# Kernel tuning notes

Measured on AMD Instinct MI355X. Metric: run time of the kernel, lower is better.

Reference implementation:

```python
import jax, jax.numpy as jnp
import numpy as np

D_MODEL = 1024
N_HEADS = 16
D_HEAD = D_MODEL // N_HEADS
B, S = 4, 2048


def setup_inputs() -> dict:
    key = jax.random.key(0)
    ks = jax.random.split(key, 12)
    std = 1.0 / np.sqrt(D_MODEL)
    inp = {
        "q": jax.random.normal(ks[0], (B, S, D_MODEL), jnp.float32),
        "k": jax.random.normal(ks[1], (B, S, D_MODEL), jnp.float32),
        "v": jax.random.normal(ks[2], (B, S, D_MODEL), jnp.float32),
        # causal mask: 1 where attention is disallowed (j > i)
        "mask": jnp.triu(jnp.ones((S, S), jnp.int32), k=1)[None, None],
        "Wq": jax.random.normal(ks[3], (D_MODEL, D_MODEL), jnp.float32) * std,
        "bq": jnp.zeros((D_MODEL,), jnp.float32),
        "Wk": jax.random.normal(ks[4], (D_MODEL, D_MODEL), jnp.float32) * std,
        "bk": jnp.zeros((D_MODEL,), jnp.float32),
        "Wv": jax.random.normal(ks[5], (D_MODEL, D_MODEL), jnp.float32) * std,
        "bv": jnp.zeros((D_MODEL,), jnp.float32),
        "Wo": jax.random.normal(ks[6], (D_MODEL, D_MODEL), jnp.float32) * std,
        "bo": jnp.zeros((D_MODEL,), jnp.float32),
    }
    return inp


def _split_heads(x):
    # [B, S, D] -> [B, H, S, d_head]
    b, s, _ = x.shape
    return x.reshape(b, s, N_HEADS, D_HEAD).transpose(0, 2, 1, 3)


def reference(q, k, v, mask, Wq, bq, Wk, bk, Wv, bv, Wo, bo):
    # torch Linear: y = x @ W.T + b
    qh = _split_heads(q @ Wq.T + bq)
    kh = _split_heads(k @ Wk.T + bk)
    vh = _split_heads(v @ Wv.T + bv)
    # NOTE: original scales by sqrt(d_model), not sqrt(d_head)
    scale = 1.0 / np.sqrt(D_MODEL).astype(np.float32)
    logits = jnp.einsum("bhqd,bhkd->bhqk", qh, kh) * scale
    logits = logits + mask.astype(logits.dtype) * (-1e9)
    weights = jax.nn.softmax(logits, axis=-1)
    attn = jnp.einsum("bhqk,bhkd->bhqd", weights, vh)
    attn = attn.transpose(0, 2, 1, 3).reshape(q.shape[0], -1, D_MODEL)
    out = attn @ Wo.T + bo
    return out, weights
```

## Files before the change

kernel.cpp:

```cpp
#include <hip/hip_runtime.h>
#include <stdint.h>

typedef unsigned short u16;
typedef __attribute__((ext_vector_type(8))) short bf16x8;
typedef __attribute__((ext_vector_type(8))) unsigned short us8;
typedef __attribute__((ext_vector_type(4))) float f32x4;

typedef __attribute__((address_space(1))) void as1_void;
typedef __attribute__((address_space(3))) void as3_void;

#define S_LEN 2048
#define DMODEL 1024
#define DH 64
#define NHEADS 16
#define NB 4
#define GM (NB * S_LEN)
#define GN DMODEL
#define GK DMODEL
#define SCALE 0.03125f

__device__ __forceinline__ void gload16(const void* g, void* l) {
  __builtin_amdgcn_global_load_lds((const as1_void*)g, (as3_void*)l, 16, 0, 0);
}
__device__ __forceinline__ float bf2f(u16 u) {
  union { unsigned int i; float f; } x; x.i = ((unsigned int)u) << 16; return x.f;
}
__device__ __forceinline__ u16 f2bf(float f) {
  union { float f; unsigned int i; } x; x.f = f;
  unsigned int u = x.i + 0x7fffu + ((x.i >> 16) & 1u);
  return (u16)(u >> 16);
}
__device__ __forceinline__ f32x4 mfma16(bf16x8 a, bf16x8 b, f32x4 c) {
  return __builtin_amdgcn_mfma_f32_16x16x32_bf16(a, b, c, 0, 0, 0);
}
__device__ __forceinline__ void nt_store4(f32x4 v, float* p) {
  __builtin_nontemporal_store(v, (f32x4*)p);
}

__device__ __forceinline__ void cvt_chunk(const float* s, u16* d, int i) {
  const f32x4 a = *(const f32x4*)(s + (size_t)i * 8);
  const f32x4 b = *(const f32x4*)(s + (size_t)i * 8 + 4);
  us8 o;
  o[0] = f2bf(a[0]); o[1] = f2bf(a[1]); o[2] = f2bf(a[2]); o[3] = f2bf(a[3]);
  o[4] = f2bf(b[0]); o[5] = f2bf(b[1]); o[6] = f2bf(b[2]); o[7] = f2bf(b[3]);
  *(us8*)(d + (size_t)i * 8) = o;
}
__global__ __launch_bounds__(256)
void cvt3(const float* __restrict__ s0, const float* __restrict__ s1,
          const float* __restrict__ s2, u16* __restrict__ d0,
          u16* __restrict__ d1, u16* __restrict__ d2, int n8) {
  const int i = blockIdx.x * 256 + threadIdx.x;
  if (i >= n8) return;
  const float* s; u16* d;
  if (blockIdx.y == 0)      { s = s0; d = d0; }
  else if (blockIdx.y == 1) { s = s1; d = d1; }
  else                      { s = s2; d = d2; }
  cvt_chunk(s, d, i);
}
__global__ __launch_bounds__(256)
void cvt4(const float* __restrict__ s0, const float* __restrict__ s1,
          const float* __restrict__ s2, const float* __restrict__ s3,
          u16* __restrict__ d0, u16* __restrict__ d1,
          u16* __restrict__ d2, u16* __restrict__ d3, int n8) {
  const int i = blockIdx.x * 256 + threadIdx.x;
  if (i >= n8) return;
  const float* s; u16* d;
  if (blockIdx.y == 0)      { s = s0; d = d0; }
  else if (blockIdx.y == 1) { s = s1; d = d1; }
  else if (blockIdx.y == 2) { s = s2; d = d2; }
  else                      { s = s3; d = d3; }
  cvt_chunk(s, d, i);
}

template<bool OUTF>
__device__ __forceinline__ void gemm_body(const u16* __restrict__ A,
                                          const u16* __restrict__ W,
                                          const float* __restrict__ bias,
                                          void* __restrict__ Cv,
                                          u16* smem) {
  u16* As = smem;
  u16* Bs = smem + 2 * 8192;
  const int tid  = threadIdx.x;
  const int lane = tid & 63;
  const int wv   = tid >> 6;
  const int wr   = wv >> 1, wc = wv & 1;
  const int rlow = lane & 15, rhi = lane >> 4;
  const int m0 = blockIdx.x * 128;
  const int n0 = blockIdx.y * 128;

  f32x4 acc[4][4];
#pragma unroll
  for (int i = 0; i < 4; ++i)
#pragma unroll
    for (int j = 0; j < 4; ++j) acc[i][j] = (f32x4){0.f, 0.f, 0.f, 0.f};

#define STAGE_G(bufi, kk)                                                     \
  {                                                                           \
    _Pragma("unroll")                                                         \
    for (int i = 0; i < 4; ++i) {                                             \
      const int c = i * 256 + tid;                                            \
      const int row = c >> 3, cw = c & 7;                                     \
      const int koff = ((kk) << 6) + ((cw ^ (row & 7)) << 3);                 \
      gload16(A + (size_t)(m0 + row) * GK + koff,                             \
              &As[(bufi) * 8192 + ((c - lane) << 3)]);                        \
      gload16(W + (size_t)(n0 + row) * GK + koff,                             \
              &Bs[(bufi) * 8192 + ((c - lane) << 3)]);                        \
    }                                                                         \
  }

  const int nk = GK >> 6;
  STAGE_G(0, 0);
  __syncthreads();
  int buf = 0;
  for (int kk = 0; kk < nk; ++kk) {
    if (kk + 1 < nk) STAGE_G(buf ^ 1, kk + 1);
    const u16* Ab = &As[buf * 8192];
    const u16* Bb = &Bs[buf * 8192];
    bf16x8 af[4][2], bfr[4][2];
#pragma unroll
    for (int mi = 0; mi < 4; ++mi) {
      const int row = wr * 64 + mi * 16 + rlow;
#pragma unroll
      for (int k2 = 0; k2 < 2; ++k2)
        af[mi][k2] = *(const bf16x8*)&Ab[row * 64 + (((rhi + k2 * 4) ^ (row & 7)) << 3)];
    }
#pragma unroll
    for (int ni = 0; ni < 4; ++ni) {
      const int row = wc * 64 + ni * 16 + rlow;
#pragma unroll
      for (int k2 = 0; k2 < 2; ++k2)
        bfr[ni][k2] = *(const bf16x8*)&Bb[row * 64 + (((rhi + k2 * 4) ^ (row & 7)) << 3)];
    }
#pragma unroll
    for (int mi = 0; mi < 4; ++mi)
#pragma unroll
      for (int ni = 0; ni < 4; ++ni) {
        acc[mi][ni] = mfma16(af[mi][0], bfr[ni][0], acc[mi][ni]);
        acc[mi][ni] = mfma16(af[mi][1], bfr[ni][1], acc[mi][ni]);
      }
    __syncthreads();
    buf ^= 1;
  }
#undef STAGE_G

  if constexpr (OUTF) {
    float* Cs = (float*)smem;
#pragma unroll
    for (int ni = 0; ni < 4; ++ni) {
      const int col = wc * 64 + ni * 16 + rlow;
      const float bv = bias[n0 + col];
#pragma unroll
      for (int mi = 0; mi < 4; ++mi)
#pragma unroll
        for (int r = 0; r < 4; ++r)
          Cs[(wr * 64 + mi * 16 + rhi * 4 + r) * 128 + col] = acc[mi][ni][r] + bv;
    }
    __syncthreads();
#pragma unroll
    for (int i = 0; i < 16; ++i) {
      const int c = i * 256 + tid;
      const int row = c >> 5, cw = c & 31;
      const f32x4 t = *(const f32x4*)&Cs[row * 128 + cw * 4];
      nt_store4(t, &((float*)Cv)[(size_t)(m0 + row) * GN + n0 + cw * 4]);
    }
  } else {
    u16* Cs = smem;
#pragma unroll
    for (int ni = 0; ni < 4; ++ni) {
      const int col = wc * 64 + ni * 16 + rlow;
      const float bv = bias[n0 + col];
#pragma unroll
      for (int mi = 0; mi < 4; ++mi)
#pragma unroll
        for (int r = 0; r < 4; ++r)
          Cs[(wr * 64 + mi * 16 + rhi * 4 + r) * 144 + col] = f2bf(acc[mi][ni][r] + bv);
    }
    __syncthreads();
#pragma unroll
    for (int i = 0; i < 8; ++i) {
      const int c = i * 256 + tid;
      const int row = c >> 4, cw = c & 15;
      const us8 t = *(const us8*)&Cs[row * 144 + cw * 8];
      *(us8*)&((u16*)Cv)[(size_t)(m0 + row) * GN + n0 + cw * 8] = t;
    }
  }
}

__global__ __launch_bounds__(256, 2)
void gemm_qkv(const u16* __restrict__ xq, const u16* __restrict__ xk,
              const u16* __restrict__ xv, const u16* __restrict__ wq,
              const u16* __restrict__ wk, const u16* __restrict__ wv,
              const float* __restrict__ bq, const float* __restrict__ bk,
              const float* __restrict__ bv, u16* __restrict__ oq,
              u16* __restrict__ ok, u16* __restrict__ ov) {
  __shared__ u16 smem[4 * 8192];
  const u16 *A, *W; const float* bias; u16* C;
  if (blockIdx.z == 0)      { A = xq; W = wq; bias = bq; C = oq; }
  else if (blockIdx.z == 1) { A = xk; W = wk; bias = bk; C = ok; }
  else                      { A = xv; W = wv; bias = bv; C = ov; }
  gemm_body<false>(A, W, bias, C, smem);
}

__global__ __launch_bounds__(256, 2)
void gemm_o(const u16* __restrict__ A, const u16* __restrict__ W,
            const float* __restrict__ bias, float* __restrict__ C) {
  __shared__ u16 smem[4 * 8192];
  gemm_body<true>(A, W, bias, C, smem);
}

__global__ __launch_bounds__(512, 4)
void attn_fused(const u16* __restrict__ qh, const u16* __restrict__ kh,
                const u16* __restrict__ vh, float* __restrict__ wout,
                u16* __restrict__ am)
{
  __shared__ u16 smem[34304];
  u16* Ws = smem;
  u16* Qs = smem;
  u16* Ks = smem + 17408;
  u16* VT = smem + 17408 + 8192;

  const int tid = threadIdx.x, lane = tid & 63, wv = tid >> 6;
  const int rlow = lane & 15, rhi = lane >> 4;
  const int idx = blockIdx.x;
  const int bh  = idx & 63;
  const int qt  = 15 - (idx >> 6);
  const int b = bh >> 4, h = bh & 15;
  const int q0 = qt << 7;
  const size_t headoff = (size_t)b * S_LEN * DMODEL + h * DH;

#pragma unroll
  for (int i = 0; i < 2; ++i) {
    const int c = i * 512 + tid;
    const int row = c >> 3, cw = c & 7;
    gload16(qh + headoff + (size_t)(q0 + row) * DMODEL + ((cw ^ (row & 7)) << 3),
            &Qs[(c - lane) << 3]);
  }
  __syncthreads();
  bf16x8 qf[2];
  {
    const int row = wv * 16 + rlow;
#pragma unroll
    for (int k2 = 0; k2 < 2; ++k2)
      qf[k2] = *(const bf16x8*)&Qs[row * 64 + (((rhi + k2 * 4) ^ (row & 7)) << 3)];
  }

  const int gi_base = q0 + wv * 16 + rhi * 4;
  float ssum[4] = {0.f, 0.f, 0.f, 0.f};

  for (int jt = 0; jt <= qt; ++jt) {
    __syncthreads();
#pragma unroll
    for (int i = 0; i < 2; ++i) {
      const int c = i * 512 + tid;
      const int row = c >> 3, cw = c & 7;
      gload16(kh + headoff + (size_t)(jt * 128 + row) * DMODEL + ((cw ^ (row & 7)) << 3),
              &Ks[(c - lane) << 3]);
    }
    __syncthreads();
    const bool diag = (jt == qt);
    float pexp[4] = {0.f, 0.f, 0.f, 0.f};
#pragma unroll
    for (int half = 0; half < 2; ++half) {
      f32x4 acc[4];
#pragma unroll
      for (int ni = 0; ni < 4; ++ni) acc[ni] = (f32x4){0.f, 0.f, 0.f, 0.f};
#pragma unroll
      for (int k2 = 0; k2 < 2; ++k2) {
#pragma unroll
        for (int ni = 0; ni < 4; ++ni) {
          const int row = (half * 4 + ni) * 16 + rlow;
          bf16x8 kf = *(const bf16x8*)&Ks[row * 64 + (((rhi + k2 * 4) ^ (row & 7)) << 3)];
          acc[ni] = mfma16(qf[k2], kf, acc[ni]);
        }
      }
#pragma unroll
      for (int ni = 0; ni < 4; ++ni) {
        const int gj = jt * 128 + (half * 4 + ni) * 16 + rlow;
#pragma unroll
        for (int r = 0; r < 4; ++r) {
          if (!diag || gj <= gi_base + r) pexp[r] += __expf(acc[ni][r] * SCALE);
        }
      }
    }
#pragma unroll
    for (int r = 0; r < 4; ++r) {
      float p = pexp[r];
      p += __shfl_xor(p, 1);
      p += __shfl_xor(p, 2);
      p += __shfl_xor(p, 4);
      p += __shfl_xor(p, 8);
      ssum[r] += p;
    }
  }
  float inv_s[4];
#pragma unroll
  for (int r = 0; r < 4; ++r) inv_s[r] = 1.f / ssum[r];

  f32x4 opv[4];
#pragma unroll
  for (int ni = 0; ni < 4; ++ni) opv[ni] = (f32x4){0.f, 0.f, 0.f, 0.f};

  for (int jt = 0; jt <= qt; ++jt) {
    __syncthreads();
#pragma unroll
    for (int i = 0; i < 2; ++i) {
      const int c = i * 512 + tid;
      const int row = c >> 3, cw = c & 7;
      gload16(kh + headoff + (size_t)(jt * 128 + row) * DMODEL + ((cw ^ (row & 7)) << 3),
              &Ks[(c - lane) << 3]);
    }
#pragma unroll
    for (int i = 0; i < 2; ++i) {
      const int c = i * 512 + tid;
      const int j = c >> 3, d0 = (c & 7) << 3;
      bf16x8 vv = *(const bf16x8*)(vh + headoff + (size_t)(jt * 128 + j) * DMODEL + d0);
#pragma unroll
      for (int e = 0; e < 8; ++e) VT[(d0 + e) * 136 + j] = (u16)vv[e];
    }
    __syncthreads();
    const bool diag = (jt == qt);
#pragma unroll
    for (int half = 0; half < 2; ++half) {
      f32x4 acc[4];
#pragma unroll
      for (int ni = 0; ni < 4; ++ni) acc[ni] = (f32x4){0.f, 0.f, 0.f, 0.f};
#pragma unroll
      for (int k2 = 0; k2 < 2; ++k2) {
#pragma unroll
        for (int ni = 0; ni < 4; ++ni) {
          const int row = (half * 4 + ni) * 16 + rlow;
          bf16x8 kf = *(const bf16x8*)&Ks[row * 64 + (((rhi + k2 * 4) ^ (row & 7)) << 3)];
          acc[ni] = mfma16(qf[k2], kf, acc[ni]);
        }
      }
#pragma unroll
      for (int ni = 0; ni < 4; ++ni) {
        const int col = (half * 4 + ni) * 16 + rlow;
        const int gj = jt * 128 + col;
#pragma unroll
        for (int r = 0; r < 4; ++r) {
          float w = 0.f;
          if (!diag || gj <= gi_base + r) w = __expf(acc[ni][r] * SCALE) * inv_s[r];
          Ws[(wv * 16 + rhi * 4 + r) * 136 + col] = f2bf(w);
        }
      }
    }
    __syncthreads();
    {
      const size_t wbase = ((size_t)bh * S_LEN + q0) * S_LEN + (size_t)jt * 128;
#pragma unroll
      for (int i = 0; i < 8; ++i) {
        const int c = i * 512 + tid;
        const int row = c >> 5, cw = c & 31;
        f32x4 t;
        t[0] = bf2f(Ws[row * 136 + cw * 4 + 0]);
        t[1] = bf2f(Ws[row * 136 + cw * 4 + 1]);
        t[2] = bf2f(Ws[row * 136 + cw * 4 + 2]);
        t[3] = bf2f(Ws[row * 136 + cw * 4 + 3]);
        nt_store4(t, wout + wbase + (size_t)row * S_LEN + cw * 4);
      }
    }
#pragma unroll
    for (int k4 = 0; k4 < 4; ++k4) {
      const bf16x8 afr = *(const bf16x8*)&Ws[(wv * 16 + rlow) * 136 + rhi * 8 + k4 * 32];
#pragma unroll
      for (int ni = 0; ni < 4; ++ni) {
        const bf16x8 vfr = *(const bf16x8*)&VT[(ni * 16 + rlow) * 136 + rhi * 8 + k4 * 32];
        opv[ni] = mfma16(afr, vfr, opv[ni]);
      }
    }
  }

  {
    const f32x4 z = {0.f, 0.f, 0.f, 0.f};
    for (int jt = qt + 1; jt < 16; ++jt) {
      const size_t wbase = ((size_t)bh * S_LEN + q0) * S_LEN + (size_t)jt * 128;
#pragma unroll
      for (int i = 0; i < 8; ++i) {
        const int c = i * 512 + tid;
        const int row = c >> 5, cw = c & 31;
        nt_store4(z, wout + wbase + (size_t)row * S_LEN + cw * 4);
      }
    }
  }

  __syncthreads();
  {
    u16* Os = smem;
#pragma unroll
    for (int ni = 0; ni < 4; ++ni)
#pragma unroll
      for (int r = 0; r < 4; ++r)
        Os[(wv * 16 + rhi * 4 + r) * 72 + ni * 16 + rlow] = f2bf(opv[ni][r]);
    __syncthreads();
#pragma unroll
    for (int i = 0; i < 2; ++i) {
      const int c = i * 512 + tid;
      const int row = c >> 3, cw = c & 7;
      const us8 t = *(const us8*)&Os[row * 72 + cw * 8];
      *(us8*)(am + headoff + (size_t)(q0 + row) * DMODEL + cw * 8) = t;
    }
  }
}

extern "C" void kernel_launch(void* const* d_in, const int* in_sizes, int n_in,
                              void* d_out, int out_size, void* d_ws, size_t ws_size,
                              hipStream_t stream) {
  const float* q  = (const float*)d_in[0];
  const float* k  = (const float*)d_in[1];
  const float* v  = (const float*)d_in[2];
  const float* Wq = (const float*)d_in[4];
  const float* bq = (const float*)d_in[5];
  const float* Wk = (const float*)d_in[6];
  const float* bk = (const float*)d_in[7];
  const float* Wv = (const float*)d_in[8];
  const float* bv = (const float*)d_in[9];
  const float* Wo = (const float*)d_in[10];
  const float* bo = (const float*)d_in[11];

  const size_t proj_elems = (size_t)NB * S_LEN * DMODEL;
  const size_t w_elems    = (size_t)DMODEL * DMODEL;
  float* out0 = (float*)d_out;
  float* wts  = out0 + proj_elems;

  u16* qh  = (u16*)d_ws;
  u16* kh  = qh + proj_elems;
  u16* vh  = kh + proj_elems;
  u16* am  = vh + proj_elems;
  u16* wco = am + proj_elems;

  u16* xq = (u16*)wts;
  u16* xk = xq + proj_elems;
  u16* xv = xk + proj_elems;
  u16* wq_ = xv + proj_elems;
  u16* wk_ = wq_ + w_elems;
  u16* wv_ = wk_ + w_elems;

  const int n8x = (int)(proj_elems / 8);
  const int n8w = (int)(w_elems / 8);

  cvt3<<<dim3(n8x / 256, 3), dim3(256), 0, stream>>>(q, k, v, xq, xk, xv, n8x);
  cvt4<<<dim3(n8w / 256, 4), dim3(256), 0, stream>>>(Wq, Wk, Wv, Wo,
                                                     wq_, wk_, wv_, wco, n8w);
  gemm_qkv<<<dim3(64, 8, 3), dim3(256), 0, stream>>>(xq, xk, xv, wq_, wk_, wv_,
                                                     bq, bk, bv, qh, kh, vh);
  attn_fused<<<dim3(1024), dim3(512), 0, stream>>>(qh, kh, vh, wts, am);
  gemm_o<<<dim3(64, 8), dim3(256), 0, stream>>>(am, wco, bo, out0);
}
```

Baseline: 360.5 us.

## Fuse fp32-to-bf16 activation conversion into QKV GEMM A-tile loading

Removes the separate cvt3 kernel that converted the q, k and v activations to bf16. The QKV GEMM now reads fp32 A tiles into registers, converts them, and writes them into the swizzled LDS buffer, with the register load prefetched ahead of the MFMA loop. This drops a full read-write pass over three 32 MB tensors and one launch. In exchange the GEMM reads twice as many A bytes from global memory, uses more registers, and fills LDS through normal stores instead of async global_load_lds.

```diff
diff --git a/kernel.cpp b/kernel.cpp
--- a/kernel.cpp
+++ b/kernel.cpp
@@ -36,27 +36,13 @@
 __device__ __forceinline__ void nt_store4(f32x4 v, float* p) {
   __builtin_nontemporal_store(v, (f32x4*)p);
 }
-
-__device__ __forceinline__ void cvt_chunk(const float* s, u16* d, int i) {
-  const f32x4 a = *(const f32x4*)(s + (size_t)i * 8);
-  const f32x4 b = *(const f32x4*)(s + (size_t)i * 8 + 4);
+__device__ __forceinline__ us8 cvt8(f32x4 a, f32x4 b) {
   us8 o;
   o[0] = f2bf(a[0]); o[1] = f2bf(a[1]); o[2] = f2bf(a[2]); o[3] = f2bf(a[3]);
   o[4] = f2bf(b[0]); o[5] = f2bf(b[1]); o[6] = f2bf(b[2]); o[7] = f2bf(b[3]);
-  *(us8*)(d + (size_t)i * 8) = o;
-}
-__global__ __launch_bounds__(256)
-void cvt3(const float* __restrict__ s0, const float* __restrict__ s1,
-          const float* __restrict__ s2, u16* __restrict__ d0,
-          u16* __restrict__ d1, u16* __restrict__ d2, int n8) {
-  const int i = blockIdx.x * 256 + threadIdx.x;
-  if (i >= n8) return;
-  const float* s; u16* d;
-  if (blockIdx.y == 0)      { s = s0; d = d0; }
-  else if (blockIdx.y == 1) { s = s1; d = d1; }
-  else                      { s = s2; d = d2; }
-  cvt_chunk(s, d, i);
-}
+  return o;
+}
+
 __global__ __launch_bounds__(256)
 void cvt4(const float* __restrict__ s0, const float* __restrict__ s1,
           const float* __restrict__ s2, const float* __restrict__ s3,
@@ -69,11 +55,13 @@
   else if (blockIdx.y == 1) { s = s1; d = d1; }
   else if (blockIdx.y == 2) { s = s2; d = d2; }
   else                      { s = s3; d = d3; }
-  cvt_chunk(s, d, i);
-}
-
-template<bool OUTF>
-__device__ __forceinline__ void gemm_body(const u16* __restrict__ A,
+  const f32x4 a = *(const f32x4*)(s + (size_t)i * 8);
+  const f32x4 b = *(const f32x4*)(s + (size_t)i * 8 + 4);
+  *(us8*)(d + (size_t)i * 8) = cvt8(a, b);
+}
+
+template<bool AF32, bool OUTF>
+__device__ __forceinline__ void gemm_body(const void* __restrict__ Av,
                                           const u16* __restrict__ W,
                                           const float* __restrict__ bias,
                                           void* __restrict__ Cv,
@@ -88,32 +76,81 @@
   const int m0 = blockIdx.x * 128;
   const int n0 = blockIdx.y * 128;
 
+  const u16*   Ab16 = (const u16*)Av;
+  const float* Af32 = (const float*)Av;
+
   f32x4 acc[4][4];
 #pragma unroll
   for (int i = 0; i < 4; ++i)
 #pragma unroll
     for (int j = 0; j < 4; ++j) acc[i][j] = (f32x4){0.f, 0.f, 0.f, 0.f};
 
-#define STAGE_G(bufi, kk)                                                     \
+#define STAGE_B16(bufi, kk)                                                   \
   {                                                                           \
     _Pragma("unroll")                                                         \
     for (int i = 0; i < 4; ++i) {                                             \
       const int c = i * 256 + tid;                                            \
       const int row = c >> 3, cw = c & 7;                                     \
       const int koff = ((kk) << 6) + ((cw ^ (row & 7)) << 3);                 \
-      gload16(A + (size_t)(m0 + row) * GK + koff,                             \
-              &As[(bufi) * 8192 + ((c - lane) << 3)]);                        \
       gload16(W + (size_t)(n0 + row) * GK + koff,                             \
               &Bs[(bufi) * 8192 + ((c - lane) << 3)]);                        \
     }                                                                         \
   }
-
+#define STAGE_A16(bufi, kk)                                                   \
+  {                                                                           \
+    _Pragma("unroll")                                                         \
+    for (int i = 0; i < 4; ++i) {                                             \
+      const int c = i * 256 + tid;                                            \
+      const int row = c >> 3, cw = c & 7;                                     \
+      const int koff = ((kk) << 6) + ((cw ^ (row & 7)) << 3);                 \
+      gload16(Ab16 + (size_t)(m0 + row) * GK + koff,                          \
+              &As[(bufi) * 8192 + ((c - lane) << 3)]);                        \
+    }                                                                         \
+  }
+#define LOAD_AF32(kk)                                                         \
+  {                                                                           \
+    _Pragma("unroll")                                                         \
+    for (int i = 0; i < 4; ++i) {                                             \
+      const int c = i * 256 + tid;                                            \
+      const int row = c >> 3, cw = c & 7;                                     \
+      const float* src = Af32 + (size_t)(m0 + row) * GK + ((kk) << 6) +       \
+                         ((cw ^ (row & 7)) << 3);                             \
+      areg0[i] = *(const f32x4*)src;                                          \
+      areg1[i] = *(const f32x4*)(src + 4);                                    \
+    }                                                                         \
+  }
+#define WRITE_AF32(bufi)                                                      \
+  {                                                                           \
+    _Pragma("unroll")                                                         \
+    for (int i = 0; i < 4; ++i) {                                             \
+      const int c = i * 256 + tid;                                            \
+      *(us8*)&As[(bufi) * 8192 + (c << 3)] = cvt8(areg0[i], areg1[i]);        \
+    }                                                                         \
+  }
+
+  f32x4 areg0[4], areg1[4];
   const int nk = GK >> 6;
-  STAGE_G(0, 0);
+
+  if constexpr (AF32) {
+    LOAD_AF32(0);
+    STAGE_B16(0, 0);
+    WRITE_AF32(0);
+  } else {
+    STAGE_A16(0, 0);
+    STAGE_B16(0, 0);
+  }
   __syncthreads();
   int buf = 0;
   for (int kk = 0; kk < nk; ++kk) {
-    if (kk + 1 < nk) STAGE_G(buf ^ 1, kk + 1);
+    if (kk + 1 < nk) {
+      if constexpr (AF32) {
+        LOAD_AF32(kk + 1);
+        STAGE_B16(buf ^ 1, kk + 1);
+      } else {
+        STAGE_A16(buf ^ 1, kk + 1);
+        STAGE_B16(buf ^ 1, kk + 1);
+      }
+    }
     const u16* Ab = &As[buf * 8192];
     const u16* Bb = &Bs[buf * 8192];
     bf16x8 af[4][2], bfr[4][2];
@@ -138,10 +175,16 @@
         acc[mi][ni] = mfma16(af[mi][0], bfr[ni][0], acc[mi][ni]);
         acc[mi][ni] = mfma16(af[mi][1], bfr[ni][1], acc[mi][ni]);
       }
+    if constexpr (AF32) {
+      if (kk + 1 < nk) WRITE_AF32(buf ^ 1);
+    }
     __syncthreads();
     buf ^= 1;
   }
-#undef STAGE_G
+#undef STAGE_B16
+#undef STAGE_A16
+#undef LOAD_AF32
+#undef WRITE_AF32
 
   if constexpr (OUTF) {
     float* Cs = (float*)smem;
@@ -187,25 +230,25 @@
 }
 
 __global__ __launch_bounds__(256, 2)
-void gemm_qkv(const u16* __restrict__ xq, const u16* __restrict__ xk,
-              const u16* __restrict__ xv, const u16* __restrict__ wq,
+void gemm_qkv(const float* __restrict__ xq, const float* __restrict__ xk,
+              const float* __restrict__ xv, const u16* __restrict__ wq,
               const u16* __restrict__ wk, const u16* __restrict__ wv,
               const float* __restrict__ bq, const float* __restrict__ bk,
               const float* __restrict__ bv, u16* __restrict__ oq,
               u16* __restrict__ ok, u16* __restrict__ ov) {
   __shared__ u16 smem[4 * 8192];
-  const u16 *A, *W; const float* bias; u16* C;
+  const float* A; const u16* W; const float* bias; u16* C;
   if (blockIdx.z == 0)      { A = xq; W = wq; bias = bq; C = oq; }
   else if (blockIdx.z == 1) { A = xk; W = wk; bias = bk; C = ok; }
   else                      { A = xv; W = wv; bias = bv; C = ov; }
-  gemm_body<false>(A, W, bias, C, smem);
+  gemm_body<true, false>(A, W, bias, C, smem);
 }
 
 __global__ __launch_bounds__(256, 2)
 void gemm_o(const u16* __restrict__ A, const u16* __restrict__ W,
             const float* __restrict__ bias, float* __restrict__ C) {
   __shared__ u16 smem[4 * 8192];
-  gemm_body<true>(A, W, bias, C, smem);
+  gemm_body<false, true>(A, W, bias, C, smem);
 }
 
 __global__ __launch_bounds__(512, 4)
@@ -429,20 +472,15 @@
   u16* am  = vh + proj_elems;
   u16* wco = am + proj_elems;
 
-  u16* xq = (u16*)wts;
-  u16* xk = xq + proj_elems;
-  u16* xv = xk + proj_elems;
-  u16* wq_ = xv + proj_elems;
+  u16* wq_ = (u16*)wts;
   u16* wk_ = wq_ + w_elems;
   u16* wv_ = wk_ + w_elems;
 
-  const int n8x = (int)(proj_elems / 8);
   const int n8w = (int)(w_elems / 8);
 
-  cvt3<<<dim3(n8x / 256, 3), dim3(256), 0, stream>>>(q, k, v, xq, xk, xv, n8x);
   cvt4<<<dim3(n8w / 256, 4), dim3(256), 0, stream>>>(Wq, Wk, Wv, Wo,
                                                      wq_, wk_, wv_, wco, n8w);
-  gemm_qkv<<<dim3(64, 8, 3), dim3(256), 0, stream>>>(xq, xk, xv, wq_, wk_, wv_,
+  gemm_qkv<<<dim3(64, 8, 3), dim3(256), 0, stream>>>(q, k, v, wq_, wk_, wv_,
                                                      bq, bk, bv, qh, kh, vh);
   attn_fused<<<dim3(1024), dim3(512), 0, stream>>>(qh, kh, vh, wts, am);
   gemm_o<<<dim3(64, 8), dim3(256), 0, stream>>>(am, wco, bo, out0);
```

Result: slower. 369.8 us (+2.6%).
